# Kernel optimization log

Measured on AMD Instinct MI355X. Metric: run time of the kernel, lower is better.

The kernel has to match this reference:

```python
import jax, jax.numpy as jnp
import numpy as np

M = 11            # memory_length
DEG = 5           # degree
K = DEG - 1       # number of polynomial orders (1..DEG-1)
WCOL = 1 + K * M  # 45
B, T = 32, 4096


def setup_inputs() -> dict:
    key = jax.random.key(0)
    kx, kw = jax.random.split(key)
    x = jax.random.normal(kx, (B, T, 2), dtype=jnp.float32)
    h_0 = jnp.zeros((1,), dtype=jnp.float32)  # unused by the module, API compat
    Weight = jax.random.normal(kw, (1, M * WCOL), dtype=jnp.float32) * 0.05
    return {"x": x, "h_0": h_0, "Weight": Weight}


def _gmp(x, Weight):
    Bb, Tt, _ = x.shape
    xc = jax.lax.complex(x[..., 0], x[..., 1])                       # (B,T) complex64
    pad = jnp.zeros((Bb, M - 1), dtype=xc.dtype)
    xp = jnp.concatenate([pad, xc], axis=1)                           # (B, T+M-1)
    amp = jnp.abs(jnp.concatenate([pad, xp], axis=1))                 # (B, T+2M-2), doubly padded as in torch code
    # powers |x|^1 .. |x|^(DEG-1)
    pows = amp[:, None, :] ** jnp.arange(1, DEG, dtype=amp.dtype)[None, :, None]  # (B,K,L)
    j = jnp.arange(Tt)
    l = jnp.arange(M)
    m = jnp.arange(M)
    # windows_x[b,j,m] = xp[b, j+m]  (m=M-1 is the current sample)
    wx = xp[:, j[:, None] + m[None, :]]                               # (B,T,M)
    # windows_degree slice in the torch loop: pow[b,k, j+l+m]
    idx = j[:, None, None] + l[None, :, None] + m[None, None, :]      # (T,M,M)
    G = pows[:, :, idx]                                               # (B,K,T,M,M) real
    W0 = Weight[0, :M]                                                # linear taps
    W1 = Weight[0, M:].reshape(K, M, M)                               # cross-term taps, (k,l,m) order = torch reshape order
    # contract the real envelope tensor with W1 first to avoid a huge complex intermediate
    S = jnp.einsum('bktlm,klm->btm', G, W1)                           # (B,T,M)
    out_c = jnp.einsum('btm,m->bt', wx, W0.astype(xc.dtype)) + jnp.sum(wx * S, axis=-1)
    return jnp.stack([jnp.real(out_c), jnp.imag(out_c)], axis=-1)     # (B,T,2) float32


def reference(x, h_0, Weight):
    # h_0 is accepted but unused, matching the torch module
    return _gmp(x, Weight)
```

## Files before the change

kernel.cpp:

```cpp
#include <hip/hip_runtime.h>


#define GMP_M 11
#define GMP_T 4096
#define GMP_B 32
#define TILE 128
#define HALO 20

__global__ __launch_bounds__(256) void gmp_kernel(const float* __restrict__ x,
                                                  const float* __restrict__ W,
                                                  float* __restrict__ out) {
    const int b   = blockIdx.y;
    const int t0  = blockIdx.x * TILE;
    const int tid = threadIdx.x;
    const int lt  = tid & (TILE - 1);
    const int half = __builtin_amdgcn_readfirstlane(tid >> 7);

    __shared__ float2 xs[TILE + HALO];
    __shared__ float2 pA[TILE + HALO];
    __shared__ float2 pB[TILE + HALO];
    __shared__ float2 psum[TILE];

    const float2* xb = (const float2*)(x + (size_t)b * GMP_T * 2);

    for (int i = tid; i < TILE + HALO; i += 256) {
        int g = t0 - HALO + i;
        float2 v = make_float2(0.f, 0.f);
        if (g >= 0) v = xb[g];
        xs[i] = v;
        float r2 = v.x * v.x + v.y * v.y;
        float a  = sqrtf(r2);
        pA[i] = make_float2(a, r2);
        pB[i] = make_float2(r2 * a, r2 * r2);
    }
    __syncthreads();

    const float2* __restrict__ pS = half ? pB : pA;
    float2 P[HALO + 1];
#pragma unroll
    for (int q = 0; q <= HALO; ++q) P[q] = pS[lt + q];

    const float* __restrict__ Wb = W + GMP_M + half * 2 * 121;

    float2 acc = make_float2(0.f, 0.f);
#pragma unroll
    for (int m = 0; m < GMP_M; ++m) {
        float gm = half ? 0.f : W[m];
#pragma unroll
        for (int l = 0; l < GMP_M; ++l) {
            float2 p = P[l + m];
            gm += p.x * Wb[0 * 121 + l * 11 + m]
                + p.y * Wb[1 * 121 + l * 11 + m];
        }
        float2 xv = xs[lt + m + (GMP_M - 1)];
        acc.x += xv.x * gm;
        acc.y += xv.y * gm;
    }

    if (half) {
        psum[lt] = acc;
    }
    __syncthreads();
    if (!half) {
        float2 o = psum[lt];
        o.x += acc.x;
        o.y += acc.y;
        float2* ob = (float2*)(out + ((size_t)b * GMP_T + t0) * 2);
        ob[lt] = o;
    }
}

extern "C" void kernel_launch(void* const* d_in, const int* in_sizes, int n_in,
                              void* d_out, int out_size, void* d_ws, size_t ws_size,
                              hipStream_t stream) {
    (void)in_sizes; (void)n_in; (void)d_ws; (void)ws_size; (void)out_size;
    const float* x = (const float*)d_in[0];
    const float* W = (const float*)d_in[2];
    float* out = (float*)d_out;

    dim3 grid(GMP_T / TILE, GMP_B, 1);
    dim3 block(256, 1, 1);
    gmp_kernel<<<grid, block, 0, stream>>>(x, W, out);
}
```

Measured before the change: 72.15 us.

## Split polynomial orders across four wavefronts with a 64-sample tile

Halves the time tile to 64 samples and assigns each of the four wavefronts in a block one polynomial order, where before each half-block took two orders. The envelope powers move to a per-order scalar shared-memory layout, and three partial sums are reduced through shared memory at the end. The aim is to double the number of blocks and shorten each thread's serial FMA chain to gain parallelism on a small problem. In exchange, more halo is loaded and recomputed per output, and the final reduction has more steps.

```diff
diff --git a/kernel.cpp b/kernel.cpp
--- a/kernel.cpp
+++ b/kernel.cpp
@@ -4,7 +4,7 @@
 #define GMP_M 11
 #define GMP_T 4096
 #define GMP_B 32
-#define TILE 128
+#define TILE 64
 #define HALO 20
 
 __global__ __launch_bounds__(256) void gmp_kernel(const float* __restrict__ x,
@@ -13,13 +13,12 @@
     const int b   = blockIdx.y;
     const int t0  = blockIdx.x * TILE;
     const int tid = threadIdx.x;
-    const int lt  = tid & (TILE - 1);
-    const int half = __builtin_amdgcn_readfirstlane(tid >> 7);
+    const int lt  = tid & 63;
+    const int q   = __builtin_amdgcn_readfirstlane(tid >> 6);
 
     __shared__ float2 xs[TILE + HALO];
-    __shared__ float2 pA[TILE + HALO];
-    __shared__ float2 pB[TILE + HALO];
-    __shared__ float2 psum[TILE];
+    __shared__ float  pk[4][TILE + HALO];
+    __shared__ float2 psum[3 * TILE];
 
     const float2* xb = (const float2*)(x + (size_t)b * GMP_T * 2);
 
@@ -30,41 +29,43 @@
         xs[i] = v;
         float r2 = v.x * v.x + v.y * v.y;
         float a  = sqrtf(r2);
-        pA[i] = make_float2(a, r2);
-        pB[i] = make_float2(r2 * a, r2 * r2);
+        pk[0][i] = a;
+        pk[1][i] = r2;
+        pk[2][i] = r2 * a;
+        pk[3][i] = r2 * r2;
     }
     __syncthreads();
 
-    const float2* __restrict__ pS = half ? pB : pA;
-    float2 P[HALO + 1];
+    float P[HALO + 1];
 #pragma unroll
-    for (int q = 0; q <= HALO; ++q) P[q] = pS[lt + q];
+    for (int s = 0; s <= HALO; ++s) P[s] = pk[q][lt + s];
 
-    const float* __restrict__ Wb = W + GMP_M + half * 2 * 121;
+    const float* __restrict__ Wb = W + GMP_M + q * 121;
 
     float2 acc = make_float2(0.f, 0.f);
 #pragma unroll
     for (int m = 0; m < GMP_M; ++m) {
-        float gm = half ? 0.f : W[m];
+        float gm = (q == 0) ? W[m] : 0.f;
 #pragma unroll
-        for (int l = 0; l < GMP_M; ++l) {
-            float2 p = P[l + m];
-            gm += p.x * Wb[0 * 121 + l * 11 + m]
-                + p.y * Wb[1 * 121 + l * 11 + m];
-        }
+        for (int l = 0; l < GMP_M; ++l)
+            gm += P[l + m] * Wb[l * 11 + m];
         float2 xv = xs[lt + m + (GMP_M - 1)];
         acc.x += xv.x * gm;
         acc.y += xv.y * gm;
     }
 
-    if (half) {
-        psum[lt] = acc;
+    if (q) {
+        psum[(q - 1) * TILE + lt] = acc;
     }
     __syncthreads();
-    if (!half) {
-        float2 o = psum[lt];
-        o.x += acc.x;
-        o.y += acc.y;
+    if (q == 0) {
+        float2 o = acc;
+#pragma unroll
+        for (int j = 0; j < 3; ++j) {
+            float2 p = psum[j * TILE + lt];
+            o.x += p.x;
+            o.y += p.y;
+        }
         float2* ob = (float2*)(out + ((size_t)b * GMP_T + t0) * 2);
         ob[lt] = o;
     }
```

New measurement: 63.31 us. -12.3%, faster.
